# Performance work log

Measured on AMD Instinct MI355X. Metric: run time of the kernel, lower is better.

Reference implementation:

```python
import jax, jax.numpy as jnp
import numpy as np

C_IN = 256
C_OUT = 256
NUM_HEADS = 4
C_HEAD = C_OUT // NUM_HEADS  # 64
ALPHA = 0.2
NEG_FILL = -9e15


def setup_inputs() -> dict:
    key = jax.random.key(0)
    k1, k2, k3, k4, k5 = jax.random.split(key, 5)
    B, N = 1, 4096
    node_feats = jax.random.normal(k1, (B, N, C_IN), dtype=jnp.float32)
    adj_matrix = jax.random.randint(k2, (B, N, N), 0, 2, dtype=jnp.int32)
    # xavier_uniform with gain=1.414 on projection weight (fan_in=C_IN, fan_out=C_OUT)
    lim_w = 1.414 * np.sqrt(6.0 / (C_IN + C_OUT))
    W = jax.random.uniform(k3, (C_IN, C_OUT), dtype=jnp.float32, minval=-lim_w, maxval=lim_w)
    b = jnp.zeros((C_OUT,), dtype=jnp.float32)
    lim_a = 1.414 * np.sqrt(6.0 / (NUM_HEADS + 2 * C_HEAD))
    a = jax.random.uniform(k4, (NUM_HEADS, 2 * C_HEAD), dtype=jnp.float32, minval=-lim_a, maxval=lim_a)
    return {"node_feats": node_feats, "adj_matrix": adj_matrix, "W": W, "b": b, "a": a}


def reference(node_feats, adj_matrix, W, b, a):
    B, N, _ = node_feats.shape
    # linear projection -> (B, N, H, C_HEAD)
    feats = (node_feats @ W + b).reshape(B, N, NUM_HEADS, C_HEAD)
    # attention logit for edge (i -> j): a_src . h_i + a_dst . h_j, per head
    a_src, a_dst = a[:, :C_HEAD], a[:, C_HEAD:]
    src = jnp.einsum('bnhc,hc->bnh', feats, a_src)  # indexed by row i
    dst = jnp.einsum('bnhc,hc->bnh', feats, a_dst)  # indexed by col j
    logits = src[:, :, None, :] + dst[:, None, :, :]  # (B, N, N, H)
    logits = jnp.where(logits >= 0, logits, ALPHA * logits)  # LeakyReLU(0.2)
    attn = jnp.where(adj_matrix[..., None] == 1, logits, NEG_FILL)
    probs = jax.nn.softmax(attn, axis=2)  # softmax over source nodes j
    out = jnp.einsum('bijh,bjhc->bihc', probs, feats)
    return out.reshape(B, N, NUM_HEADS * C_HEAD)  # concat heads
```

## Files before the change

kernel.cpp:

```cpp
#include <hip/hip_runtime.h>

#define NN 4096
#define C 256
#define NH 4
#define CH 64
#define JSPLIT 8
#define JSLICE (NN / JSPLIT)
#define NJT (JSLICE / 32)

typedef float f32x4 __attribute__((ext_vector_type(4)));
typedef __bf16 b16x8 __attribute__((ext_vector_type(8)));
typedef unsigned short u16x8 __attribute__((ext_vector_type(8)));
typedef unsigned int u32x4 __attribute__((ext_vector_type(4)));

__device__ inline float fast_exp2(float x) {
#if __has_builtin(__builtin_amdgcn_exp2f)
  return __builtin_amdgcn_exp2f(x);
#else
  return exp2f(x);
#endif
}

__device__ inline unsigned pack2bf(float f0, float f1) {
  unsigned u0 = __float_as_uint(f0) + 0x8000u;
  unsigned u1 = __float_as_uint(f1) + 0x8000u;
  return __builtin_amdgcn_perm(u1, u0, 0x07060302u);
}

__global__ __launch_bounds__(256) void k_prep(
    const int* __restrict__ adj, const float* __restrict__ X,
    const float* __restrict__ W, unsigned char* __restrict__ packed,
    unsigned short* __restrict__ Xbf, unsigned short* __restrict__ WT) {
  const int b = blockIdx.x, t = threadIdx.x;
  if (b < 8192) {
    const int idx = b * 256 + t;
    const int4 a0 = *(const int4*)(adj + (size_t)idx * 8);
    const int4 a1 = *(const int4*)(adj + (size_t)idx * 8 + 4);
    unsigned m = 0;
    m |= (a0.x != 0) ? 1u : 0u;   m |= (a0.y != 0) ? 2u : 0u;
    m |= (a0.z != 0) ? 4u : 0u;   m |= (a0.w != 0) ? 8u : 0u;
    m |= (a1.x != 0) ? 16u : 0u;  m |= (a1.y != 0) ? 32u : 0u;
    m |= (a1.z != 0) ? 64u : 0u;  m |= (a1.w != 0) ? 128u : 0u;
    packed[idx] = (unsigned char)m;
  } else if (b < 9216) {
    const int idx = (b - 8192) * 256 + t;
    const float4 v = ((const float4*)X)[idx];
    uint2 st;
    st.x = pack2bf(v.x, v.y);
    st.y = pack2bf(v.z, v.w);
    ((uint2*)Xbf)[idx] = st;
  } else {
    const int c = b - 9216;
    const float w = W[(size_t)t * C + c];
    WT[(size_t)c * C + t] = (unsigned short)((__float_as_uint(w) + 0x8000u) >> 16);
  }
}

__global__ __launch_bounds__(256) void k_feats(
    const unsigned short* __restrict__ Xbf, const unsigned short* __restrict__ WT,
    const float* __restrict__ bias, const float* __restrict__ av,
    unsigned short* __restrict__ F, float* __restrict__ srcv,
    float2* __restrict__ dstT2) {
  const int i0 = blockIdx.x * 16;
  const int h = threadIdx.x >> 6;
  const int lane = threadIdx.x & 63;
  const int q = lane >> 4, n = lane & 15;
  const int c0 = h * CH;
  const float LOG2E = 1.4426950408889634f;

  const f32x4 zero = {0.f, 0.f, 0.f, 0.f};
  f32x4 acc[4];
#pragma unroll
  for (int g = 0; g < 4; ++g) acc[g] = zero;

  const unsigned short* ap = Xbf + (size_t)(i0 + n) * C + q * 8;
#pragma unroll
  for (int kt = 0; kt < 8; ++kt) {
    const b16x8 aF = __builtin_bit_cast(b16x8, *(const u16x8*)(ap + kt * 32));
#pragma unroll
    for (int g = 0; g < 4; ++g) {
      const b16x8 bF = __builtin_bit_cast(b16x8,
          *(const u16x8*)(WT + (size_t)(c0 + g * 16 + n) * C + kt * 32 + q * 8));
      acc[g] = __builtin_amdgcn_mfma_f32_16x16x32_bf16(aF, bF, acc[g], 0, 0, 0);
    }
  }

  float fb[4][4], asv[4], adv[4];
#pragma unroll
  for (int g = 0; g < 4; ++g) {
    const float bs = bias[c0 + g * 16 + n];
    asv[g] = av[h * 128 + g * 16 + n];
    adv[g] = av[h * 128 + 64 + g * 16 + n];
#pragma unroll
    for (int r = 0; r < 4; ++r) fb[g][r] = acc[g][r] + bs;
  }
  const int jt = i0 >> 5, half = (i0 >> 4) & 1;
  const int qp = half * 2 + (q >> 1);
#pragma unroll
  for (int g = 0; g < 4; ++g) {
    uint2 st;
    st.x = pack2bf(fb[g][0], fb[g][1]);
    st.y = pack2bf(fb[g][2], fb[g][3]);
    *(uint2*)(F + ((size_t)((jt * NH + h) * 4 + g)) * 512 + (qp * 16 + n) * 8 + 4 * (q & 1)) = st;
  }
#pragma unroll
  for (int r = 0; r < 4; ++r) {
    float p = 0.f, d = 0.f;
#pragma unroll
    for (int g = 0; g < 4; ++g) {
      p = fmaf(fb[g][r], asv[g], p);
      d = fmaf(fb[g][r], adv[g], d);
    }
#pragma unroll
    for (int m = 1; m < 16; m <<= 1) {
      p += __shfl_xor(p, m);
      d += __shfl_xor(d, m);
    }
    if (n == 0) {
      const int row = i0 + q * 4 + r;
      srcv[(size_t)row * NH + h] = p;
      const float dL = d * LOG2E;
      dstT2[(size_t)h * NN + row] = make_float2(dL, 0.2f * dL);
    }
  }
}

__global__ __launch_bounds__(256, 4) void k_attn(
    const unsigned char* __restrict__ packed,
    const unsigned short* __restrict__ F,
    const float* __restrict__ srcv, const float2* __restrict__ dstT2,
    _Float16* __restrict__ pacc, float* __restrict__ lpart) {
  const int slice = blockIdx.x;
  const int i0 = blockIdx.y * 32;
  const int h = threadIdx.x >> 6;
  const int lane = threadIdx.x & 63;
  const int q = lane >> 4, n = lane & 15;
  const int jbase = slice * JSLICE;

  const float LOG2E = 1.4426950408889634f;
  const int r0 = i0 + n, r1 = i0 + 16 + n;
  const float s0 = srcv[(size_t)r0 * NH + h];
  const float s1 = srcv[(size_t)r1 * NH + h];
  const float xm0 = s0 + 16.0f, xm1 = s1 + 16.0f;
  const float m20 = fmaxf(xm0, 0.2f * xm0) * LOG2E;
  const float m21 = fmaxf(xm1, 0.2f * xm1) * LOG2E;
  const float u0 = fmaf(s0, LOG2E, -m20), w0 = fmaf(0.2f * s0, LOG2E, -m20);
  const float u1 = fmaf(s1, LOG2E, -m21), w1 = fmaf(0.2f * s1, LOG2E, -m21);

  const f32x4 zero = {0.f, 0.f, 0.f, 0.f};
  f32x4 acc0[4], acc1[4], lacc0 = zero, lacc1 = zero;
#pragma unroll
  for (int g = 0; g < 4; ++g) { acc0[g] = zero; acc1[g] = zero; }

  u16x8 ou;
#pragma unroll
  for (int jj = 0; jj < 8; ++jj) ou[jj] = 0x3F80;
  const b16x8 ones = __builtin_bit_cast(b16x8, ou);

  const u32x4 m40 = *(const u32x4*)(packed + (size_t)r0 * 512 + (jbase >> 3) + q * 16);
  const u32x4 m41 = *(const u32x4*)(packed + (size_t)r1 * 512 + (jbase >> 3) + q * 16);

  const float* dp2 = (const float*)(dstT2 + (size_t)h * NN + jbase);
  const unsigned short* fp = F + ((size_t)((jbase >> 5) * NH + h) * 4) * 512 + lane * 8;

#pragma unroll
  for (int a = 0; a < 4; ++a) {
#pragma unroll
    for (int b = 0; b < 4; ++b) {
      const int jt = a * 4 + b;
      b16x8 bF[4];
#pragma unroll
      for (int g = 0; g < 4; ++g)
        bF[g] = __builtin_bit_cast(b16x8,
            *(const u16x8*)(fp + (size_t)(jt * NH * 4 + g) * 512));

      const unsigned Mb0 = (unsigned(__shfl((int)m40[b], a * 16 + n)) >> (q * 8)) & 0xffu;
      const unsigned Mb1 = (unsigned(__shfl((int)m41[b], a * 16 + n)) >> (q * 8)) & 0xffu;

      const float* dq = dp2 + jt * 64 + q * 16;
      const float4 dd0 = *(const float4*)(dq);
      const float4 dd1 = *(const float4*)(dq + 4);
      const float4 dd2 = *(const float4*)(dq + 8);
      const float4 dd3 = *(const float4*)(dq + 12);
      const float4 dd[4] = {dd0, dd1, dd2, dd3};

      u32x4 pk0, pk1;
#pragma unroll
      for (int k = 0; k < 4; ++k) {
        const float a00 = fmaxf(dd[k].x + u0, dd[k].y + w0);
        const float a01 = fmaxf(dd[k].z + u0, dd[k].w + w0);
        const float a10 = fmaxf(dd[k].x + u1, dd[k].y + w1);
        const float a11 = fmaxf(dd[k].z + u1, dd[k].w + w1);
        const float e00 = fast_exp2((Mb0 & (1u << (2 * k))) ? a00 : -200.0f);
        const float e01 = fast_exp2((Mb0 & (2u << (2 * k))) ? a01 : -200.0f);
        const float e10 = fast_exp2((Mb1 & (1u << (2 * k))) ? a10 : -200.0f);
        const float e11 = fast_exp2((Mb1 & (2u << (2 * k))) ? a11 : -200.0f);
        pk0[k] = pack2bf(e00, e01);
        pk1[k] = pack2bf(e10, e11);
      }
      const b16x8 E0 = __builtin_bit_cast(b16x8, pk0);
      const b16x8 E1 = __builtin_bit_cast(b16x8, pk1);
#pragma unroll
      for (int g = 0; g < 4; ++g) {
        acc0[g] = __builtin_amdgcn_mfma_f32_16x16x32_bf16(E0, bF[g], acc0[g], 0, 0, 0);
        acc1[g] = __builtin_amdgcn_mfma_f32_16x16x32_bf16(E1, bF[g], acc1[g], 0, 0, 0);
      }
      lacc0 = __builtin_amdgcn_mfma_f32_16x16x32_bf16(E0, ones, lacc0, 0, 0, 0);
      lacc1 = __builtin_amdgcn_mfma_f32_16x16x32_bf16(E1, ones, lacc1, 0, 0, 0);
    }
  }

#pragma unroll
  for (int g = 0; g < 4; ++g)
#pragma unroll
    for (int r = 0; r < 4; ++r) {
      const int col = h * CH + g * 16 + n;
      pacc[((size_t)slice * NN + i0 + q * 4 + r) * C + col] = (_Float16)acc0[g][r];
      pacc[((size_t)slice * NN + i0 + 16 + q * 4 + r) * C + col] = (_Float16)acc1[g][r];
    }
  if (n == 0) {
#pragma unroll
    for (int r = 0; r < 4; ++r) {
      lpart[((size_t)slice * NN + i0 + q * 4 + r) * NH + h] = lacc0[r];
      lpart[((size_t)slice * NN + i0 + 16 + q * 4 + r) * NH + h] = lacc1[r];
    }
  }
}

__global__ __launch_bounds__(256) void k_final(
    const _Float16* __restrict__ pacc, const float* __restrict__ lpart,
    float* __restrict__ out) {
  const int i = blockIdx.x;
  const int c = threadIdx.x;
  const int h = c >> 6;
  float l = 0.f, sa = 0.f;
#pragma unroll
  for (int sp = 0; sp < JSPLIT; ++sp) {
    l += lpart[((size_t)sp * NN + i) * NH + h];
    sa += (float)pacc[((size_t)sp * NN + i) * C + c];
  }
  out[(size_t)i * C + c] = sa / l;
}

extern "C" void kernel_launch(void* const* d_in, const int* in_sizes, int n_in,
                              void* d_out, int out_size, void* d_ws, size_t ws_size,
                              hipStream_t stream) {
  const float* nf   = (const float*)d_in[0];
  const int* adj    = (const int*)d_in[1];
  const float* W    = (const float*)d_in[2];
  const float* bias = (const float*)d_in[3];
  const float* av   = (const float*)d_in[4];
  float* out = (float*)d_out;

  char* ws = (char*)d_ws;
  unsigned char* packed  = (unsigned char*)ws;
  unsigned short* Xbf    = (unsigned short*)(ws + (2u << 20));
  unsigned short* WT     = (unsigned short*)(ws + (4u << 20));
  unsigned short* F      = (unsigned short*)(ws + (4u << 20) + (256u << 10));
  float* srcv   = (float*)(ws + (6u << 20) + (256u << 10));
  float2* dstT2 = (float2*)(ws + (6u << 20) + (320u << 10));
  float* lpart  = (float*)(ws + (6u << 20) + (448u << 10));
  _Float16* pacc = (_Float16*)(ws + (8u << 20));

  k_prep<<<9472, 256, 0, stream>>>(adj, nf, W, packed, Xbf, WT);
  k_feats<<<NN / 16, 256, 0, stream>>>(Xbf, WT, bias, av, F, srcv, dstT2);
  dim3 g2(JSPLIT, NN / 32);
  k_attn<<<g2, 256, 0, stream>>>(packed, F, srcv, dstT2, pacc, lpart);
  k_final<<<NN, 256, 0, stream>>>(pacc, lpart, out);
}
```

Baseline: 141.6 us.

## Read adjacency directly in attention and factor the exponential into precomputed products

Drops the separate adjacency bit-packing pass. The attention kernel now reads the int32 adjacency rows directly, which removes a full pass over the adjacency data and its intermediate buffer. It also rewrites exp(leaky(s+d)) as the max of two products of exponentials precomputed per row and per column, so the inner loop uses multiplies instead of exp2 per edge. The cost is that each warp per head re-reads the same adjacency rows, and the precomputed exponentials risk overflow or underflow when logits are large.

```diff
diff --git a/kernel.cpp b/kernel.cpp
--- a/kernel.cpp
+++ b/kernel.cpp
@@ -28,29 +28,18 @@
 }
 
 __global__ __launch_bounds__(256) void k_prep(
-    const int* __restrict__ adj, const float* __restrict__ X,
-    const float* __restrict__ W, unsigned char* __restrict__ packed,
+    const float* __restrict__ X, const float* __restrict__ W,
     unsigned short* __restrict__ Xbf, unsigned short* __restrict__ WT) {
   const int b = blockIdx.x, t = threadIdx.x;
-  if (b < 8192) {
+  if (b < 1024) {
     const int idx = b * 256 + t;
-    const int4 a0 = *(const int4*)(adj + (size_t)idx * 8);
-    const int4 a1 = *(const int4*)(adj + (size_t)idx * 8 + 4);
-    unsigned m = 0;
-    m |= (a0.x != 0) ? 1u : 0u;   m |= (a0.y != 0) ? 2u : 0u;
-    m |= (a0.z != 0) ? 4u : 0u;   m |= (a0.w != 0) ? 8u : 0u;
-    m |= (a1.x != 0) ? 16u : 0u;  m |= (a1.y != 0) ? 32u : 0u;
-    m |= (a1.z != 0) ? 64u : 0u;  m |= (a1.w != 0) ? 128u : 0u;
-    packed[idx] = (unsigned char)m;
-  } else if (b < 9216) {
-    const int idx = (b - 8192) * 256 + t;
     const float4 v = ((const float4*)X)[idx];
     uint2 st;
     st.x = pack2bf(v.x, v.y);
     st.y = pack2bf(v.z, v.w);
     ((uint2*)Xbf)[idx] = st;
   } else {
-    const int c = b - 9216;
+    const int c = b - 1024;
     const float w = W[(size_t)t * C + c];
     WT[(size_t)c * C + t] = (unsigned short)((__float_as_uint(w) + 0x8000u) >> 16);
   }
@@ -59,8 +48,8 @@
 __global__ __launch_bounds__(256) void k_feats(
     const unsigned short* __restrict__ Xbf, const unsigned short* __restrict__ WT,
     const float* __restrict__ bias, const float* __restrict__ av,
-    unsigned short* __restrict__ F, float* __restrict__ srcv,
-    float2* __restrict__ dstT2) {
+    unsigned short* __restrict__ F, float2* __restrict__ srcAB,
+    float2* __restrict__ EdT2) {
   const int i0 = blockIdx.x * 16;
   const int h = threadIdx.x >> 6;
   const int lane = threadIdx.x & 63;
@@ -118,17 +107,21 @@
     }
     if (n == 0) {
       const int row = i0 + q * 4 + r;
-      srcv[(size_t)row * NH + h] = p;
       const float dL = d * LOG2E;
-      dstT2[(size_t)h * NN + row] = make_float2(dL, 0.2f * dL);
+      EdT2[(size_t)h * NN + row] = make_float2(fast_exp2(dL), fast_exp2(0.2f * dL));
+      const float x = p + 16.0f;
+      const float m2 = fmaxf(x, 0.2f * x) * LOG2E;
+      srcAB[(size_t)row * NH + h] = make_float2(
+          fast_exp2(fmaf(p, LOG2E, -m2)),
+          fast_exp2(fmaf(0.2f * p, LOG2E, -m2)));
     }
   }
 }
 
 __global__ __launch_bounds__(256, 4) void k_attn(
-    const unsigned char* __restrict__ packed,
+    const int* __restrict__ adj,
     const unsigned short* __restrict__ F,
-    const float* __restrict__ srcv, const float2* __restrict__ dstT2,
+    const float2* __restrict__ srcAB, const float2* __restrict__ EdT2,
     _Float16* __restrict__ pacc, float* __restrict__ lpart) {
   const int slice = blockIdx.x;
   const int i0 = blockIdx.y * 32;
@@ -137,15 +130,9 @@
   const int q = lane >> 4, n = lane & 15;
   const int jbase = slice * JSLICE;
 
-  const float LOG2E = 1.4426950408889634f;
   const int r0 = i0 + n, r1 = i0 + 16 + n;
-  const float s0 = srcv[(size_t)r0 * NH + h];
-  const float s1 = srcv[(size_t)r1 * NH + h];
-  const float xm0 = s0 + 16.0f, xm1 = s1 + 16.0f;
-  const float m20 = fmaxf(xm0, 0.2f * xm0) * LOG2E;
-  const float m21 = fmaxf(xm1, 0.2f * xm1) * LOG2E;
-  const float u0 = fmaf(s0, LOG2E, -m20), w0 = fmaf(0.2f * s0, LOG2E, -m20);
-  const float u1 = fmaf(s1, LOG2E, -m21), w1 = fmaf(0.2f * s1, LOG2E, -m21);
+  const float2 ab0 = srcAB[(size_t)r0 * NH + h];
+  const float2 ab1 = srcAB[(size_t)r1 * NH + h];
 
   const f32x4 zero = {0.f, 0.f, 0.f, 0.f};
   f32x4 acc0[4], acc1[4], lacc0 = zero, lacc1 = zero;
@@ -157,10 +144,9 @@
   for (int jj = 0; jj < 8; ++jj) ou[jj] = 0x3F80;
   const b16x8 ones = __builtin_bit_cast(b16x8, ou);
 
-  const u32x4 m40 = *(const u32x4*)(packed + (size_t)r0 * 512 + (jbase >> 3) + q * 16);
-  const u32x4 m41 = *(const u32x4*)(packed + (size_t)r1 * 512 + (jbase >> 3) + q * 16);
-
-  const float* dp2 = (const float*)(dstT2 + (size_t)h * NN + jbase);
+  const int* aj0 = adj + (size_t)r0 * NN + jbase + q * 8;
+  const int* aj1 = adj + (size_t)r1 * NN + jbase + q * 8;
+  const float* dp2 = (const float*)(EdT2 + (size_t)h * NN + jbase);
   const unsigned short* fp = F + ((size_t)((jbase >> 5) * NH + h) * 4) * 512 + lane * 8;
 
 #pragma unroll
@@ -174,8 +160,12 @@
         bF[g] = __builtin_bit_cast(b16x8,
             *(const u16x8*)(fp + (size_t)(jt * NH * 4 + g) * 512));
 
-      const unsigned Mb0 = (unsigned(__shfl((int)m40[b], a * 16 + n)) >> (q * 8)) & 0xffu;
-      const unsigned Mb1 = (unsigned(__shfl((int)m41[b], a * 16 + n)) >> (q * 8)) & 0xffu;
+      const int4 M0a = *(const int4*)(aj0 + jt * 32);
+      const int4 M0b = *(const int4*)(aj0 + jt * 32 + 4);
+      const int4 M1a = *(const int4*)(aj1 + jt * 32);
+      const int4 M1b = *(const int4*)(aj1 + jt * 32 + 4);
+      const int m0[8] = {M0a.x, M0a.y, M0a.z, M0a.w, M0b.x, M0b.y, M0b.z, M0b.w};
+      const int m1[8] = {M1a.x, M1a.y, M1a.z, M1a.w, M1b.x, M1b.y, M1b.z, M1b.w};
 
       const float* dq = dp2 + jt * 64 + q * 16;
       const float4 dd0 = *(const float4*)(dq);
@@ -187,14 +177,11 @@
       u32x4 pk0, pk1;
 #pragma unroll
       for (int k = 0; k < 4; ++k) {
-        const float a00 = fmaxf(dd[k].x + u0, dd[k].y + w0);
-        const float a01 = fmaxf(dd[k].z + u0, dd[k].w + w0);
-        const float a10 = fmaxf(dd[k].x + u1, dd[k].y + w1);
-        const float a11 = fmaxf(dd[k].z + u1, dd[k].w + w1);
-        const float e00 = fast_exp2((Mb0 & (1u << (2 * k))) ? a00 : -200.0f);
-        const float e01 = fast_exp2((Mb0 & (2u << (2 * k))) ? a01 : -200.0f);
-        const float e10 = fast_exp2((Mb1 & (1u << (2 * k))) ? a10 : -200.0f);
-        const float e11 = fast_exp2((Mb1 & (2u << (2 * k))) ? a11 : -200.0f);
+        const float4 d = dd[k];
+        const float e00 = m0[2 * k]     ? fmaxf(d.x * ab0.x, d.y * ab0.y) : 0.f;
+        const float e01 = m0[2 * k + 1] ? fmaxf(d.z * ab0.x, d.w * ab0.y) : 0.f;
+        const float e10 = m1[2 * k]     ? fmaxf(d.x * ab1.x, d.y * ab1.y) : 0.f;
+        const float e11 = m1[2 * k + 1] ? fmaxf(d.z * ab1.x, d.w * ab1.y) : 0.f;
         pk0[k] = pack2bf(e00, e01);
         pk1[k] = pack2bf(e10, e11);
       }
@@ -253,18 +240,17 @@
   float* out = (float*)d_out;
 
   char* ws = (char*)d_ws;
-  unsigned char* packed  = (unsigned char*)ws;
-  unsigned short* Xbf    = (unsigned short*)(ws + (2u << 20));
-  unsigned short* WT     = (unsigned short*)(ws + (4u << 20));
-  unsigned short* F      = (unsigned short*)(ws + (4u << 20) + (256u << 10));
-  float* srcv   = (float*)(ws + (6u << 20) + (256u << 10));
-  float2* dstT2 = (float2*)(ws + (6u << 20) + (320u << 10));
-  float* lpart  = (float*)(ws + (6u << 20) + (448u << 10));
+  unsigned short* Xbf = (unsigned short*)ws;
+  unsigned short* WT  = (unsigned short*)(ws + (2u << 20));
+  unsigned short* F   = (unsigned short*)(ws + (2u << 20) + (128u << 10));
+  float2* srcAB = (float2*)(ws + (4u << 20) + (128u << 10));
+  float2* EdT2  = (float2*)(ws + (4u << 20) + (256u << 10));
+  float* lpart  = (float*)(ws + (4u << 20) + (384u << 10));
   _Float16* pacc = (_Float16*)(ws + (8u << 20));
 
-  k_prep<<<9472, 256, 0, stream>>>(adj, nf, W, packed, Xbf, WT);
-  k_feats<<<NN / 16, 256, 0, stream>>>(Xbf, WT, bias, av, F, srcv, dstT2);
+  k_prep<<<1280, 256, 0, stream>>>(nf, W, Xbf, WT);
+  k_feats<<<NN / 16, 256, 0, stream>>>(Xbf, WT, bias, av, F, srcAB, EdT2);
   dim3 g2(JSPLIT, NN / 32);
-  k_attn<<<g2, 256, 0, stream>>>(packed, F, srcv, dstT2, pacc, lpart);
+  k_attn<<<g2, 256, 0, stream>>>(adj, F, srcAB, EdT2, pacc, lpart);
   k_final<<<NN, 256, 0, stream>>>(pacc, lpart, out);
 }
```

Result: slower. 160.3 us (+13.2%).
